# Kernel optimization log

Measured on AMD Instinct MI355X. Metric: run time of the kernel, lower is better.

The kernel has to match this reference:

```python
import jax, jax.numpy as jnp
import numpy as np

N_NODES = 50000

# DGL ChebConv with k=2 and the standard lambda_max=2 approximation:
#   L_hat = L - I = -D^{-1/2} A D^{-1/2}
#   X0 = X ; X1 = L_hat @ X ; out = concat([X0, X1], -1) @ W + b
# Norm uses in-degrees (DGL behavior).

def setup_inputs() -> dict:
    key = jax.random.key(0)
    ks = jax.random.split(key, 8)
    E = 800000
    src = jax.random.randint(ks[0], (E,), 0, N_NODES, dtype=jnp.int32)
    dst = jax.random.randint(ks[1], (E,), 0, N_NODES, dtype=jnp.int32)
    def w(k, shape):
        fan_in = shape[0]
        return jax.random.normal(k, shape, jnp.float32) * (1.0 / np.sqrt(fan_in))
    return {
        "x": jax.random.normal(ks[2], (N_NODES, 128), jnp.float32),
        "src": src, "dst": dst,
        "W1": w(ks[3], (256, 256)), "b1": jnp.zeros((256,), jnp.float32),
        "W2": w(ks[4], (512, 256)), "b2": jnp.zeros((256,), jnp.float32),
        "W3": w(ks[5], (512, 128)), "b3": jnp.zeros((128,), jnp.float32),
    }

def _cheb_layer(h, src, dst, dinv, W, b):
    # X1 = -D^{-1/2} A D^{-1/2} h  (lambda_max = 2)
    hn = h * dinv[:, None]
    agg = jax.ops.segment_sum(hn[src], dst, num_segments=N_NODES)
    x1 = -(agg * dinv[:, None])
    return jnp.concatenate([h, x1], axis=-1) @ W + b

def reference(x, src, dst, W1, b1, W2, b2, W3, b3):
    deg = jax.ops.segment_sum(jnp.ones_like(dst, dtype=x.dtype), dst,
                              num_segments=N_NODES)
    dinv = jnp.where(deg > 0, jax.lax.rsqrt(jnp.maximum(deg, 1.0)), 0.0)
    h = jnp.tanh(_cheb_layer(x, src, dst, dinv, W1, b1))
    for _ in range(3):  # hid_layer = 3
        h = jnp.tanh(_cheb_layer(h, src, dst, dinv, W2, b2))
    return _cheb_layer(h, src, dst, dinv, W3, b3)
```

## Files before the change

### kernel.cpp

```cpp
#include <hip/hip_runtime.h>
#include <cmath>

#define NN 50000

typedef short v8s __attribute__((ext_vector_type(8)));
typedef float v4f __attribute__((ext_vector_type(4)));

__device__ __forceinline__ float b2f(unsigned short u) {
    return __uint_as_float(((unsigned int)u) << 16);
}
__device__ __forceinline__ unsigned short f2b(float f) {
    unsigned int x = __float_as_uint(f);
    x += 0x7fffu + ((x >> 16) & 1u);
    return (unsigned short)(x >> 16);
}

__device__ __forceinline__ void gld16(const void* g, void* l) {
    __builtin_amdgcn_global_load_lds(
        (const __attribute__((address_space(1))) unsigned int*)g,
        (__attribute__((address_space(3))) unsigned int*)l, 16, 0, 0);
}

__global__ void sniff_kernel(const unsigned short* __restrict__ x, int* __restrict__ mode) {
    if (threadIdx.x == 0 && blockIdx.x == 0) {
        int c = 0;
        for (int i = 0; i < 128; ++i) {
            unsigned int e = (x[i] >> 7) & 0xFFu;
            if (e >= 100u && e <= 140u) ++c;
        }
        *mode = (c >= 112) ? 0 : 1;
    }
}

__global__ void deg_kernel(const int* __restrict__ dst, int* __restrict__ deg, int E) {
    int e = blockIdx.x * blockDim.x + threadIdx.x;
    if (e < E) atomicAdd(&deg[dst[e]], 1);
}

__global__ void part_kernel(const int* __restrict__ deg, int* __restrict__ part, int n) {
    __shared__ int sm[256];
    int t = threadIdx.x;
    int base = blockIdx.x * 1024 + t * 4;
    int s = 0;
    if (base + 3 < n) {
        int4 v = *(const int4*)(deg + base);
        s = v.x + v.y + v.z + v.w;
    } else {
        for (int i = 0; i < 4; ++i) if (base + i < n) s += deg[base + i];
    }
    sm[t] = s;
    __syncthreads();
    for (int off = 128; off > 0; off >>= 1) {
        if (t < off) sm[t] += sm[t + off];
        __syncthreads();
    }
    if (t == 0) part[blockIdx.x] = sm[0];
}

__global__ void partscan_kernel(int* __restrict__ part, int nb, int* __restrict__ total_out) {
    int t = threadIdx.x;
    int orig = (t < nb) ? part[t] : 0;
    int v = orig;
    for (int off = 1; off < 64; off <<= 1) {
        int u = __shfl_up(v, off, 64);
        if (t >= off) v += u;
    }
    if (t < nb) part[t] = v - orig;
    if (t == 63) *total_out = v;
}

__global__ void scan2_kernel(const int* __restrict__ deg, const int* __restrict__ part,
                             int* __restrict__ row_ptr, int* __restrict__ cursor,
                             float* __restrict__ dinv, int n) {
    __shared__ int sm[256];
    int t = threadIdx.x;
    int base = blockIdx.x * 1024 + t * 4;
    int d[4]; int s = 0;
#pragma unroll
    for (int i = 0; i < 4; ++i) { d[i] = (base + i < n) ? deg[base + i] : 0; s += d[i]; }
    sm[t] = s;
    __syncthreads();
    for (int off = 1; off < 256; off <<= 1) {
        int u = (t >= off) ? sm[t - off] : 0;
        __syncthreads();
        sm[t] += u;
        __syncthreads();
    }
    int run = part[blockIdx.x] + sm[t] - s;
#pragma unroll
    for (int i = 0; i < 4; ++i) {
        int idx = base + i;
        if (idx < n) {
            row_ptr[idx] = run;
            cursor[idx]  = run;
            dinv[idx]    = (d[i] > 0) ? rsqrtf((float)d[i]) : 0.0f;
            run += d[i];
        }
    }
}

__global__ void fill_kernel(const int* __restrict__ src, const int* __restrict__ dst,
                            int* __restrict__ cursor, int* __restrict__ csr, int E) {
    int e = blockIdx.x * blockDim.x + threadIdx.x;
    if (e < E) {
        int d = dst[e];
        int pos = atomicAdd(&cursor[d], 1);
        csr[pos] = src[e];
    }
}

__global__ void transpose_kernel(const void* __restrict__ W, unsigned short* __restrict__ WT,
                                 int K, int F, const int* __restrict__ modep) {
    int mode = *modep;
    int tid = blockIdx.x * blockDim.x + threadIdx.x;
    if (tid < K * F) {
        int n = tid / K, k = tid % K;
        unsigned short v = mode ? f2b(((const float*)W)[k * F + n])
                                : ((const unsigned short*)W)[k * F + n];
        WT[tid] = v;
    }
}

__global__ void cvt_kernel(const void* __restrict__ in, unsigned short* __restrict__ out,
                           int n, const int* __restrict__ modep) {
    int mode = *modep;
    int i = blockIdx.x * blockDim.x + threadIdx.x;
    if (i < n) out[i] = mode ? f2b(((const float*)in)[i]) : ((const unsigned short*)in)[i];
}

__global__ void pack_kernel(const void* __restrict__ x, unsigned short* __restrict__ buf,
                            const int* __restrict__ modep) {
    int mode = *modep;
    int tid = blockIdx.x * blockDim.x + threadIdx.x;
    if (tid < NN * 16) {
        int n = tid >> 4, c = tid & 15;
        if (mode == 0) {
            ((uint4*)buf)[n * 64 + c] = ((const uint4*)x)[n * 16 + c];
        } else {
            const float* xf = (const float*)x + (size_t)n * 128 + c * 8;
            unsigned short o[8];
#pragma unroll
            for (int i = 0; i < 8; ++i) o[i] = f2b(xf[i]);
            *(uint4*)&buf[(size_t)n * 512 + c * 8] = *(const uint4*)o;
        }
    }
}

template <int FPL>
__global__ void spmm_kernel(const unsigned short* __restrict__ h, int ldh,
                            const int* __restrict__ row_ptr, const int* __restrict__ csr,
                            const float* __restrict__ dinv,
                            unsigned short* __restrict__ out, int ldo) {
    int node = blockIdx.x * 4 + (threadIdx.x >> 6);
    int lane = threadIdx.x & 63;
    int beg = row_ptr[node], end = row_ptr[node + 1];
    float acc[FPL];
#pragma unroll
    for (int i = 0; i < FPL; ++i) acc[i] = 0.f;
    const int col = lane * FPL;

    for (int base = beg; base < end; base += 64) {
        int cnt = min(64, end - base);
        int idx = base + lane;
        int sl = csr[(idx < end) ? idx : base];
        float dl = dinv[sl];
        int g = 0;
        for (; g + 8 <= cnt; g += 8) {
            int s[8]; float d[8];
#pragma unroll
            for (int i = 0; i < 8; ++i) { s[i] = __shfl(sl, g + i); d[i] = __shfl(dl, g + i); }
            if (FPL == 4) {
                ushort4 v[8];
#pragma unroll
                for (int i = 0; i < 8; ++i)
                    v[i] = *(const ushort4*)(h + (size_t)s[i] * ldh + col);
#pragma unroll
                for (int i = 0; i < 8; ++i) {
                    acc[0] += d[i] * b2f(v[i].x); acc[1] += d[i] * b2f(v[i].y);
                    acc[2] += d[i] * b2f(v[i].z); acc[3] += d[i] * b2f(v[i].w);
                }
            } else {
                ushort2 v[8];
#pragma unroll
                for (int i = 0; i < 8; ++i)
                    v[i] = *(const ushort2*)(h + (size_t)s[i] * ldh + col);
#pragma unroll
                for (int i = 0; i < 8; ++i) {
                    acc[0] += d[i] * b2f(v[i].x); acc[1] += d[i] * b2f(v[i].y);
                }
            }
        }
        for (; g < cnt; ++g) {
            int sg = __shfl(sl, g);
            float dg = __shfl(dl, g);
            const unsigned short* hp = h + (size_t)sg * ldh + col;
            if (FPL == 4) {
                ushort4 v = *(const ushort4*)hp;
                acc[0] += dg * b2f(v.x); acc[1] += dg * b2f(v.y);
                acc[2] += dg * b2f(v.z); acc[3] += dg * b2f(v.w);
            } else {
                ushort2 v = *(const ushort2*)hp;
                acc[0] += dg * b2f(v.x); acc[1] += dg * b2f(v.y);
            }
        }
    }

    float dn = -dinv[node];
    unsigned short* op = out + (size_t)node * ldo + col;
    if (FPL == 4) {
        ushort4 o;
        o.x = f2b(acc[0] * dn); o.y = f2b(acc[1] * dn);
        o.z = f2b(acc[2] * dn); o.w = f2b(acc[3] * dn);
        *(ushort4*)op = o;
    } else {
        ushort2 o;
        o.x = f2b(acc[0] * dn); o.y = f2b(acc[1] * dn);
        *(ushort2*)op = o;
    }
}

template <int K32, int NTPW>
__global__ void gemm_lds_kernel(const unsigned short* __restrict__ A, int lda,
                                const unsigned short* __restrict__ WT,
                                const unsigned short* __restrict__ bias,
                                void* __restrict__ out, int ldo,
                                int M, int dotanh, int is_final, const int* __restrict__ modep) {
    constexpr int K  = K32 * 32;
    constexpr int NB = 4 * NTPW * 16;
    constexpr int ACHUNK = 64 * 32 * 2 / 16;
    constexpr int BCHUNK = NB * 32 * 2 / 16;
    constexpr int ROUNDS = (ACHUNK + BCHUNK) / 256;
    __shared__ unsigned short lds[(64 + NB) * 32];

    const int tid = threadIdx.x;
    const int wave = tid >> 6, lane = tid & 63, quad = lane >> 4, l16 = lane & 15;
    const int m0 = blockIdx.x * 64;

    v4f acc[4][NTPW];
#pragma unroll
    for (int mi = 0; mi < 4; ++mi)
#pragma unroll
        for (int ni = 0; ni < NTPW; ++ni) acc[mi][ni] = (v4f){0.f, 0.f, 0.f, 0.f};

    const unsigned short* gp[ROUNDS];
#pragma unroll
    for (int r = 0; r < ROUNDS; ++r) {
        int c = tid + r * 256;
        if (c < ACHUNK) {
            int row = m0 + (c >> 2);
            if (row >= M) row = M - 1;
            gp[r] = A + (size_t)row * lda + (c & 3) * 8;
        } else {
            int cb = c - ACHUNK;
            gp[r] = WT + (size_t)(cb >> 2) * K + (cb & 3) * 8;
        }
    }

    const unsigned short* aT = lds;
    const unsigned short* bT = lds + 64 * 32;

    for (int k0 = 0; k0 < K; k0 += 32) {
#pragma unroll
        for (int r = 0; r < ROUNDS; ++r) {
            int c = tid + r * 256;
            gld16(gp[r] + k0, (void*)&lds[c * 8]);
        }
        __syncthreads();

        v8s a_frag[4], b_frag[NTPW];
#pragma unroll
        for (int mi = 0; mi < 4; ++mi)
            a_frag[mi] = *(const v8s*)&aT[(mi * 16 + l16) * 32 + quad * 8];
#pragma unroll
        for (int ni = 0; ni < NTPW; ++ni)
            b_frag[ni] = *(const v8s*)&bT[(wave * NTPW * 16 + ni * 16 + l16) * 32 + quad * 8];
#pragma unroll
        for (int mi = 0; mi < 4; ++mi)
#pragma unroll
            for (int ni = 0; ni < NTPW; ++ni)
                acc[mi][ni] = __builtin_amdgcn_mfma_f32_16x16x32_bf16(a_frag[mi], b_frag[ni],
                                                                      acc[mi][ni], 0, 0, 0);
        __syncthreads();
    }

    int fin = is_final ? *modep : 0;
#pragma unroll
    for (int ni = 0; ni < NTPW; ++ni) {
        int colc = wave * NTPW * 16 + ni * 16 + l16;
        float bv = b2f(bias[colc]);
#pragma unroll
        for (int mi = 0; mi < 4; ++mi) {
#pragma unroll
            for (int r = 0; r < 4; ++r) {
                int row = m0 + mi * 16 + quad * 4 + r;
                if (row < M) {
                    float v = acc[mi][ni][r] + bv;
                    if (dotanh) v = tanhf(v);
                    if (fin) ((float*)out)[(size_t)row * ldo + colc] = v;
                    else     ((unsigned short*)out)[(size_t)row * ldo + colc] = f2b(v);
                }
            }
        }
    }
}

static inline size_t al256(size_t x) { return (x + 255) & ~(size_t)255; }

extern "C" void kernel_launch(void* const* d_in, const int* in_sizes, int n_in,
                              void* d_out, int out_size, void* d_ws, size_t ws_size,
                              hipStream_t stream) {
    const void* x  = d_in[0];
    const int* src = (const int*)d_in[1];
    const int* dst = (const int*)d_in[2];
    const void* W1 = d_in[3]; const void* b1 = d_in[4];
    const void* W2 = d_in[5]; const void* b2 = d_in[6];
    const void* W3 = d_in[7]; const void* b3 = d_in[8];
    const int E = in_sizes[1];

    char* p = (char*)d_ws;
    int* mode     = (int*)p;            p += 256;
    int* deg      = (int*)p;            p += al256((size_t)NN * 4);
    int* row_ptr  = (int*)p;            p += al256((size_t)(NN + 1) * 4);
    int* cursor   = (int*)p;            p += al256((size_t)NN * 4);
    float* dinv   = (float*)p;          p += al256((size_t)NN * 4);
    int* part     = (int*)p;            p += al256((size_t)64 * 4);
    int* csr      = (int*)p;            p += al256((size_t)E * 4);
    unsigned short* WT1 = (unsigned short*)p; p += al256((size_t)256 * 256 * 2);
    unsigned short* WT2 = (unsigned short*)p; p += al256((size_t)256 * 512 * 2);
    unsigned short* WT3 = (unsigned short*)p; p += al256((size_t)128 * 512 * 2);
    unsigned short* bb1 = (unsigned short*)p; p += al256((size_t)256 * 2);
    unsigned short* bb2 = (unsigned short*)p; p += al256((size_t)256 * 2);
    unsigned short* bb3 = (unsigned short*)p; p += al256((size_t)128 * 2);
    unsigned short* buf = (unsigned short*)p; p += al256((size_t)NN * 512 * 2);

    hipMemsetAsync(deg, 0, (size_t)NN * 4, stream);
    sniff_kernel<<<1, 64, 0, stream>>>((const unsigned short*)x, mode);

    int eb = (E + 255) / 256;
    const int SB = (NN + 1023) / 1024;
    deg_kernel<<<eb, 256, 0, stream>>>(dst, deg, E);
    part_kernel<<<SB, 256, 0, stream>>>(deg, part, NN);
    partscan_kernel<<<1, 64, 0, stream>>>(part, SB, row_ptr + NN);
    scan2_kernel<<<SB, 256, 0, stream>>>(deg, part, row_ptr, cursor, dinv, NN);
    fill_kernel<<<eb, 256, 0, stream>>>(src, dst, cursor, csr, E);

    transpose_kernel<<<(256 * 256 + 255) / 256, 256, 0, stream>>>(W1, WT1, 256, 256, mode);
    transpose_kernel<<<(512 * 256 + 255) / 256, 256, 0, stream>>>(W2, WT2, 512, 256, mode);
    transpose_kernel<<<(512 * 128 + 255) / 256, 256, 0, stream>>>(W3, WT3, 512, 128, mode);
    cvt_kernel<<<1, 256, 0, stream>>>(b1, bb1, 256, mode);
    cvt_kernel<<<1, 256, 0, stream>>>(b2, bb2, 256, mode);
    cvt_kernel<<<1, 256, 0, stream>>>(b3, bb3, 128, mode);
    pack_kernel<<<(NN * 16 + 255) / 256, 256, 0, stream>>>(x, buf, mode);

    const int SPMM_GRID = NN / 4;
    const int GB = (NN + 63) / 64;

    spmm_kernel<2><<<SPMM_GRID, 256, 0, stream>>>(buf, 512, row_ptr, csr, dinv, buf + 128, 512);
    gemm_lds_kernel<8, 4><<<GB, 256, 0, stream>>>(buf, 512, WT1, bb1, buf, 512, NN, 1, 0, mode);
    spmm_kernel<4><<<SPMM_GRID, 256, 0, stream>>>(buf, 512, row_ptr, csr, dinv, buf + 256, 512);
    gemm_lds_kernel<16, 4><<<GB, 256, 0, stream>>>(buf, 512, WT2, bb2, buf, 512, NN, 1, 0, mode);
    spmm_kernel<4><<<SPMM_GRID, 256, 0, stream>>>(buf, 512, row_ptr, csr, dinv, buf + 256, 512);
    gemm_lds_kernel<16, 4><<<GB, 256, 0, stream>>>(buf, 512, WT2, bb2, buf, 512, NN, 1, 0, mode);
    spmm_kernel<4><<<SPMM_GRID, 256, 0, stream>>>(buf, 512, row_ptr, csr, dinv, buf + 256, 512);
    gemm_lds_kernel<16, 4><<<GB, 256, 0, stream>>>(buf, 512, WT2, bb2, buf, 512, NN, 1, 0, mode);
    spmm_kernel<4><<<SPMM_GRID, 256, 0, stream>>>(buf, 512, row_ptr, csr, dinv, buf + 256, 512);
    gemm_lds_kernel<16, 2><<<GB, 256, 0, stream>>>(buf, 512, WT3, bb3, d_out, 128, NN, 0, 1, mode);
}
```

Before: 620.8 us.

## Bucket CSR neighbors by source range, use 16-bit indices, retile GEMM to 128 rows

CSR construction now counts and fills edges per (destination, source-octant) bucket, so each row's neighbor list is grouped by source range. The aim is better cache locality for the feature gathers in the SpMM. Column indices are stored as 16-bit values to halve index traffic, which works only because the node count fits in 16 bits. The degree, scan and partition buffers grow sixteenfold, so preprocessing costs more. Separately, the hidden-layer GEMMs move to 128-row tiles with 512-thread blocks and 4x4 MFMA tiles per wave, for more operand reuse per LDS load.

```diff
diff --git a/kernel.cpp b/kernel.cpp
--- a/kernel.cpp
+++ b/kernel.cpp
@@ -2,6 +2,8 @@
 #include <cmath>
 
 #define NN 50000
+#define NOCT 16
+#define OCTW 3125
 
 typedef short v8s __attribute__((ext_vector_type(8)));
 typedef float v4f __attribute__((ext_vector_type(4)));
@@ -32,9 +34,13 @@
     }
 }
 
-__global__ void deg_kernel(const int* __restrict__ dst, int* __restrict__ deg, int E) {
+__global__ void deg_kernel(const int* __restrict__ src, const int* __restrict__ dst,
+                           int* __restrict__ deg2, int E) {
     int e = blockIdx.x * blockDim.x + threadIdx.x;
-    if (e < E) atomicAdd(&deg[dst[e]], 1);
+    if (e < E) {
+        unsigned int oct = (unsigned int)src[e] / OCTW;
+        atomicAdd(&deg2[dst[e] * NOCT + oct], 1);
+    }
 }
 
 __global__ void part_kernel(const int* __restrict__ deg, int* __restrict__ part, int n) {
@@ -57,21 +63,34 @@
     if (t == 0) part[blockIdx.x] = sm[0];
 }
 
-__global__ void partscan_kernel(int* __restrict__ part, int nb, int* __restrict__ total_out) {
+__global__ void partscan_kernel(int* __restrict__ part, int nb) {
+    __shared__ int sm[256];
     int t = threadIdx.x;
-    int orig = (t < nb) ? part[t] : 0;
-    int v = orig;
-    for (int off = 1; off < 64; off <<= 1) {
-        int u = __shfl_up(v, off, 64);
-        if (t >= off) v += u;
-    }
-    if (t < nb) part[t] = v - orig;
-    if (t == 63) *total_out = v;
+    int v[4]; int s = 0;
+#pragma unroll
+    for (int i = 0; i < 4; ++i) {
+        int idx = t * 4 + i;
+        v[i] = (idx < nb) ? part[idx] : 0;
+        s += v[i];
+    }
+    sm[t] = s;
+    __syncthreads();
+    for (int off = 1; off < 256; off <<= 1) {
+        int u = (t >= off) ? sm[t - off] : 0;
+        __syncthreads();
+        sm[t] += u;
+        __syncthreads();
+    }
+    int run = sm[t] - s;
+#pragma unroll
+    for (int i = 0; i < 4; ++i) {
+        int idx = t * 4 + i;
+        if (idx < nb) { part[idx] = run; run += v[i]; }
+    }
 }
 
 __global__ void scan2_kernel(const int* __restrict__ deg, const int* __restrict__ part,
-                             int* __restrict__ row_ptr, int* __restrict__ cursor,
-                             float* __restrict__ dinv, int n) {
+                             int* __restrict__ row_ptr, int* __restrict__ cursor, int n) {
     __shared__ int sm[256];
     int t = threadIdx.x;
     int base = blockIdx.x * 1024 + t * 4;
@@ -93,19 +112,28 @@
         if (idx < n) {
             row_ptr[idx] = run;
             cursor[idx]  = run;
-            dinv[idx]    = (d[i] > 0) ? rsqrtf((float)d[i]) : 0.0f;
             run += d[i];
-        }
+            if (idx == n - 1) row_ptr[n] = run;
+        }
+    }
+}
+
+__global__ void dinv_kernel(const int* __restrict__ rp2, float* __restrict__ dinv, int n) {
+    int i = blockIdx.x * blockDim.x + threadIdx.x;
+    if (i < n) {
+        int d = rp2[i * NOCT + NOCT] - rp2[i * NOCT];
+        dinv[i] = (d > 0) ? rsqrtf((float)d) : 0.0f;
     }
 }
 
 __global__ void fill_kernel(const int* __restrict__ src, const int* __restrict__ dst,
-                            int* __restrict__ cursor, int* __restrict__ csr, int E) {
+                            int* __restrict__ cursor, unsigned short* __restrict__ csr, int E) {
     int e = blockIdx.x * blockDim.x + threadIdx.x;
     if (e < E) {
-        int d = dst[e];
-        int pos = atomicAdd(&cursor[d], 1);
-        csr[pos] = src[e];
+        int sv = src[e];
+        unsigned int oct = (unsigned int)sv / OCTW;
+        int pos = atomicAdd(&cursor[dst[e] * NOCT + oct], 1);
+        csr[pos] = (unsigned short)sv;
     }
 }
 
@@ -148,12 +176,12 @@
 
 template <int FPL>
 __global__ void spmm_kernel(const unsigned short* __restrict__ h, int ldh,
-                            const int* __restrict__ row_ptr, const int* __restrict__ csr,
+                            const int* __restrict__ rp2, const unsigned short* __restrict__ csr,
                             const float* __restrict__ dinv,
                             unsigned short* __restrict__ out, int ldo) {
     int node = blockIdx.x * 4 + (threadIdx.x >> 6);
     int lane = threadIdx.x & 63;
-    int beg = row_ptr[node], end = row_ptr[node + 1];
+    int beg = rp2[node * NOCT], end = rp2[node * NOCT + NOCT];
     float acc[FPL];
 #pragma unroll
     for (int i = 0; i < FPL; ++i) acc[i] = 0.f;
@@ -162,7 +190,7 @@
     for (int base = beg; base < end; base += 64) {
         int cnt = min(64, end - base);
         int idx = base + lane;
-        int sl = csr[(idx < end) ? idx : base];
+        int sl = (int)csr[(idx < end) ? idx : base];
         float dl = dinv[sl];
         int g = 0;
         for (; g + 8 <= cnt; g += 8) {
@@ -219,65 +247,67 @@
     }
 }
 
-template <int K32, int NTPW>
+template <int K32, int NQ>
 __global__ void gemm_lds_kernel(const unsigned short* __restrict__ A, int lda,
                                 const unsigned short* __restrict__ WT,
                                 const unsigned short* __restrict__ bias,
                                 void* __restrict__ out, int ldo,
                                 int M, int dotanh, int is_final, const int* __restrict__ modep) {
-    constexpr int K  = K32 * 32;
-    constexpr int NB = 4 * NTPW * 16;
-    constexpr int ACHUNK = 64 * 32 * 2 / 16;
-    constexpr int BCHUNK = NB * 32 * 2 / 16;
-    constexpr int ROUNDS = (ACHUNK + BCHUNK) / 256;
-    __shared__ unsigned short lds[(64 + NB) * 32];
+    constexpr int K    = K32 * 32;
+    constexpr int NB   = NQ * 64;
+    constexpr int NTHR = 2 * NQ * 64;
+    constexpr int ACH  = 128 * 4;
+    constexpr int BCH  = NB * 4;
+    constexpr int ROUNDS = (ACH + BCH) / NTHR;
+    __shared__ unsigned short lds[(128 + NB) * 32];
 
     const int tid = threadIdx.x;
     const int wave = tid >> 6, lane = tid & 63, quad = lane >> 4, l16 = lane & 15;
-    const int m0 = blockIdx.x * 64;
-
-    v4f acc[4][NTPW];
+    const int mh = wave / NQ, nq = wave % NQ;
+    const int m0 = blockIdx.x * 128;
+
+    v4f acc[4][4];
 #pragma unroll
     for (int mi = 0; mi < 4; ++mi)
 #pragma unroll
-        for (int ni = 0; ni < NTPW; ++ni) acc[mi][ni] = (v4f){0.f, 0.f, 0.f, 0.f};
+        for (int ni = 0; ni < 4; ++ni) acc[mi][ni] = (v4f){0.f, 0.f, 0.f, 0.f};
 
     const unsigned short* gp[ROUNDS];
 #pragma unroll
     for (int r = 0; r < ROUNDS; ++r) {
-        int c = tid + r * 256;
-        if (c < ACHUNK) {
+        int c = tid + r * NTHR;
+        if (c < ACH) {
             int row = m0 + (c >> 2);
             if (row >= M) row = M - 1;
             gp[r] = A + (size_t)row * lda + (c & 3) * 8;
         } else {
-            int cb = c - ACHUNK;
+            int cb = c - ACH;
             gp[r] = WT + (size_t)(cb >> 2) * K + (cb & 3) * 8;
         }
     }
 
     const unsigned short* aT = lds;
-    const unsigned short* bT = lds + 64 * 32;
+    const unsigned short* bT = lds + 128 * 32;
 
     for (int k0 = 0; k0 < K; k0 += 32) {
 #pragma unroll
         for (int r = 0; r < ROUNDS; ++r) {
-            int c = tid + r * 256;
+            int c = tid + r * NTHR;
             gld16(gp[r] + k0, (void*)&lds[c * 8]);
         }
         __syncthreads();
 
-        v8s a_frag[4], b_frag[NTPW];
+        v8s a_frag[4], b_frag[4];
 #pragma unroll
         for (int mi = 0; mi < 4; ++mi)
-            a_frag[mi] = *(const v8s*)&aT[(mi * 16 + l16) * 32 + quad * 8];
-#pragma unroll
-        for (int ni = 0; ni < NTPW; ++ni)
-            b_frag[ni] = *(const v8s*)&bT[(wave * NTPW * 16 + ni * 16 + l16) * 32 + quad * 8];
+            a_frag[mi] = *(const v8s*)&aT[(mh * 64 + mi * 16 + l16) * 32 + quad * 8];
+#pragma unroll
+        for (int ni = 0; ni < 4; ++ni)
+            b_frag[ni] = *(const v8s*)&bT[(nq * 64 + ni * 16 + l16) * 32 + quad * 8];
 #pragma unroll
         for (int mi = 0; mi < 4; ++mi)
 #pragma unroll
-            for (int ni = 0; ni < NTPW; ++ni)
+            for (int ni = 0; ni < 4; ++ni)
                 acc[mi][ni] = __builtin_amdgcn_mfma_f32_16x16x32_bf16(a_frag[mi], b_frag[ni],
                                                                       acc[mi][ni], 0, 0, 0);
         __syncthreads();
@@ -285,14 +315,14 @@
 
     int fin = is_final ? *modep : 0;
 #pragma unroll
-    for (int ni = 0; ni < NTPW; ++ni) {
-        int colc = wave * NTPW * 16 + ni * 16 + l16;
+    for (int ni = 0; ni < 4; ++ni) {
+        int colc = nq * 64 + ni * 16 + l16;
         float bv = b2f(bias[colc]);
 #pragma unroll
         for (int mi = 0; mi < 4; ++mi) {
 #pragma unroll
             for (int r = 0; r < 4; ++r) {
-                int row = m0 + mi * 16 + quad * 4 + r;
+                int row = m0 + mh * 64 + mi * 16 + quad * 4 + r;
                 if (row < M) {
                     float v = acc[mi][ni][r] + bv;
                     if (dotanh) v = tanhf(v);
@@ -316,15 +346,15 @@
     const void* W2 = d_in[5]; const void* b2 = d_in[6];
     const void* W3 = d_in[7]; const void* b3 = d_in[8];
     const int E = in_sizes[1];
+    const int NK = NN * NOCT;
 
     char* p = (char*)d_ws;
     int* mode     = (int*)p;            p += 256;
-    int* deg      = (int*)p;            p += al256((size_t)NN * 4);
-    int* row_ptr  = (int*)p;            p += al256((size_t)(NN + 1) * 4);
-    int* cursor   = (int*)p;            p += al256((size_t)NN * 4);
+    int* deg2     = (int*)p;            p += al256((size_t)NK * 4);
+    int* rp2      = (int*)p;            p += al256((size_t)(NK + 1) * 4);
     float* dinv   = (float*)p;          p += al256((size_t)NN * 4);
-    int* part     = (int*)p;            p += al256((size_t)64 * 4);
-    int* csr      = (int*)p;            p += al256((size_t)E * 4);
+    int* part     = (int*)p;            p += al256((size_t)1024 * 4);
+    unsigned short* csr = (unsigned short*)p; p += al256((size_t)E * 2);
     unsigned short* WT1 = (unsigned short*)p; p += al256((size_t)256 * 256 * 2);
     unsigned short* WT2 = (unsigned short*)p; p += al256((size_t)256 * 512 * 2);
     unsigned short* WT3 = (unsigned short*)p; p += al256((size_t)128 * 512 * 2);
@@ -333,16 +363,17 @@
     unsigned short* bb3 = (unsigned short*)p; p += al256((size_t)128 * 2);
     unsigned short* buf = (unsigned short*)p; p += al256((size_t)NN * 512 * 2);
 
-    hipMemsetAsync(deg, 0, (size_t)NN * 4, stream);
+    hipMemsetAsync(deg2, 0, (size_t)NK * 4, stream);
     sniff_kernel<<<1, 64, 0, stream>>>((const unsigned short*)x, mode);
 
     int eb = (E + 255) / 256;
-    const int SB = (NN + 1023) / 1024;
-    deg_kernel<<<eb, 256, 0, stream>>>(dst, deg, E);
-    part_kernel<<<SB, 256, 0, stream>>>(deg, part, NN);
-    partscan_kernel<<<1, 64, 0, stream>>>(part, SB, row_ptr + NN);
-    scan2_kernel<<<SB, 256, 0, stream>>>(deg, part, row_ptr, cursor, dinv, NN);
-    fill_kernel<<<eb, 256, 0, stream>>>(src, dst, cursor, csr, E);
+    const int SB = (NK + 1023) / 1024;
+    deg_kernel<<<eb, 256, 0, stream>>>(src, dst, deg2, E);
+    part_kernel<<<SB, 256, 0, stream>>>(deg2, part, NK);
+    partscan_kernel<<<1, 256, 0, stream>>>(part, SB);
+    scan2_kernel<<<SB, 256, 0, stream>>>(deg2, part, rp2, deg2 , NK);
+    dinv_kernel<<<(NN + 255) / 256, 256, 0, stream>>>(rp2, dinv, NN);
+    fill_kernel<<<eb, 256, 0, stream>>>(src, dst, deg2 , csr, E);
 
     transpose_kernel<<<(256 * 256 + 255) / 256, 256, 0, stream>>>(W1, WT1, 256, 256, mode);
     transpose_kernel<<<(512 * 256 + 255) / 256, 256, 0, stream>>>(W2, WT2, 512, 256, mode);
@@ -353,16 +384,16 @@
     pack_kernel<<<(NN * 16 + 255) / 256, 256, 0, stream>>>(x, buf, mode);
 
     const int SPMM_GRID = NN / 4;
-    const int GB = (NN + 63) / 64;
-
-    spmm_kernel<2><<<SPMM_GRID, 256, 0, stream>>>(buf, 512, row_ptr, csr, dinv, buf + 128, 512);
-    gemm_lds_kernel<8, 4><<<GB, 256, 0, stream>>>(buf, 512, WT1, bb1, buf, 512, NN, 1, 0, mode);
-    spmm_kernel<4><<<SPMM_GRID, 256, 0, stream>>>(buf, 512, row_ptr, csr, dinv, buf + 256, 512);
-    gemm_lds_kernel<16, 4><<<GB, 256, 0, stream>>>(buf, 512, WT2, bb2, buf, 512, NN, 1, 0, mode);
-    spmm_kernel<4><<<SPMM_GRID, 256, 0, stream>>>(buf, 512, row_ptr, csr, dinv, buf + 256, 512);
-    gemm_lds_kernel<16, 4><<<GB, 256, 0, stream>>>(buf, 512, WT2, bb2, buf, 512, NN, 1, 0, mode);
-    spmm_kernel<4><<<SPMM_GRID, 256, 0, stream>>>(buf, 512, row_ptr, csr, dinv, buf + 256, 512);
-    gemm_lds_kernel<16, 4><<<GB, 256, 0, stream>>>(buf, 512, WT2, bb2, buf, 512, NN, 1, 0, mode);
-    spmm_kernel<4><<<SPMM_GRID, 256, 0, stream>>>(buf, 512, row_ptr, csr, dinv, buf + 256, 512);
+    const int GB = (NN + 127) / 128;
+
+    spmm_kernel<2><<<SPMM_GRID, 256, 0, stream>>>(buf, 512, rp2, csr, dinv, buf + 128, 512);
+    gemm_lds_kernel<8, 4><<<GB, 512, 0, stream>>>(buf, 512, WT1, bb1, buf, 512, NN, 1, 0, mode);
+    spmm_kernel<4><<<SPMM_GRID, 256, 0, stream>>>(buf, 512, rp2, csr, dinv, buf + 256, 512);
+    gemm_lds_kernel<16, 4><<<GB, 512, 0, stream>>>(buf, 512, WT2, bb2, buf, 512, NN, 1, 0, mode);
+    spmm_kernel<4><<<SPMM_GRID, 256, 0, stream>>>(buf, 512, rp2, csr, dinv, buf + 256, 512);
+    gemm_lds_kernel<16, 4><<<GB, 512, 0, stream>>>(buf, 512, WT2, bb2, buf, 512, NN, 1, 0, mode);
+    spmm_kernel<4><<<SPMM_GRID, 256, 0, stream>>>(buf, 512, rp2, csr, dinv, buf + 256, 512);
+    gemm_lds_kernel<16, 4><<<GB, 512, 0, stream>>>(buf, 512, WT2, bb2, buf, 512, NN, 1, 0, mode);
+    spmm_kernel<4><<<SPMM_GRID, 256, 0, stream>>>(buf, 512, rp2, csr, dinv, buf + 256, 512);
     gemm_lds_kernel<16, 2><<<GB, 256, 0, stream>>>(buf, 512, WT3, bb3, d_out, 128, NN, 0, 1, mode);
 }
```

After: 623.1 us. No clear change (+0.4%).
